# Performance work log

Measured on AMD Instinct MI355X. Metric: run time of the kernel, lower is better.

Reference implementation:

```python
import jax, jax.numpy as jnp
import numpy as np

B = 8        # number of clouds
NP = 4096    # points per cloud
STRIDE = 4   # sampler stride -> NS = NP // STRIDE sampled centers per cloud
K = 32       # knn neighbours
NS = NP // STRIDE


def setup_inputs() -> dict:
    key = jax.random.key(0)
    k1, k2, k3, k4 = jax.random.split(key, 4)
    N = B * NP
    x = jax.random.normal(k1, (N, 64), dtype=jnp.float32)
    pos = jax.random.normal(k2, (N, 3), dtype=jnp.float32)
    batch = jnp.repeat(jnp.arange(B, dtype=jnp.int64), NP)
    d_in = 64 + 3
    W1 = jax.random.normal(k3, (d_in, 128), dtype=jnp.float32) / np.sqrt(d_in)
    b1 = jnp.zeros((128,), dtype=jnp.float32)
    W2 = jax.random.normal(k4, (128, 256), dtype=jnp.float32) / np.sqrt(128)
    b2 = jnp.zeros((256,), dtype=jnp.float32)
    return {"x": x, "pos": pos, "batch": batch, "W1": W1, "b1": b1, "W2": W2, "b2": b2}


def reference(x, pos, batch, W1, b1, W2, b2):
    # --- sampler: stride sampling per cloud (clouds are equal-sized, contiguous) ---
    pos_b = pos.reshape(B, NP, 3)
    idx_local = jnp.arange(0, NP, STRIDE)                       # [NS]
    idx = (idx_local[None, :] + jnp.arange(B)[:, None] * NP).reshape(-1)  # global sampled idx [B*NS]
    pos_s = pos_b[:, idx_local]                                 # [B, NS, 3]

    # --- neighbour_finder: knn within each cloud (batch-respecting via per-cloud blocks) ---
    # squared distances [B, NS, NP] without materializing [B,NS,NP,3]
    d2 = ((pos_s ** 2).sum(-1)[:, :, None]
          + (pos_b ** 2).sum(-1)[:, None, :]
          - 2.0 * jnp.einsum('bsd,bnd->bsn', pos_s, pos_b))
    _, nbr = jax.lax.top_k(-d2, K)                              # [B, NS, K] local neighbour idx
    col = (nbr + (jnp.arange(B) * NP)[:, None, None]).reshape(-1)  # global neighbour idx [E]

    # --- conv: PointNetConv -> MLP(concat(x_j, pos_j - pos_i)) then max over neighbours ---
    x_j = x[col].reshape(B, NS, K, -1)                          # [B, NS, K, 64]
    rel = pos[col].reshape(B, NS, K, 3) - pos_s[:, :, None, :]  # pos_j - pos_i
    feat = jnp.concatenate([x_j, rel], axis=-1)                 # [B, NS, K, 67]
    h = jax.nn.relu(feat @ W1 + b1)                             # [B, NS, K, 128]
    h = jax.nn.relu(h @ W2 + b2)                                # [B, NS, K, 256]
    x_out = h.max(axis=2).reshape(B * NS, -1)                   # [B*NS, 256]

    pos_out = pos_s.reshape(-1, 3)
    batch_out = batch[idx]
    return x_out, pos_out, batch_out, idx
```

## Files before the change

### kernel.cpp

```cpp
#include <hip/hip_runtime.h>
#include <hip/hip_bf16.h>

#define BB 8
#define NP 4096
#define STRIDE 4
#define KNN 32
#define NS (NP/STRIDE)
#define NQ (BB*NS)
#define DIN 67
#define H1N 128
#define H2N 256
#define WCAP 512

typedef __attribute__((ext_vector_type(8)))  short bf16x8;
typedef __attribute__((ext_vector_type(16))) float f32x16;
typedef __attribute__((ext_vector_type(8)))  short short8;

__device__ __forceinline__ unsigned int f2u(float f) {
    unsigned int b = __float_as_uint(f);
    return (b & 0x80000000u) ? ~b : (b | 0x80000000u);
}
__device__ __forceinline__ short f2bf(float f) {
    unsigned u = __float_as_uint(f);
    unsigned r = u + 0x7FFFu + ((u >> 16) & 1u);
    return (short)(r >> 16);
}

__global__ __launch_bounds__(256) void knn_kernel(const float* __restrict__ pos,
                                                  int* __restrict__ col,
                                                  float* __restrict__ out) {
    __shared__ __align__(16) unsigned long long surv[4 * WCAP];
    __shared__ unsigned int pvt[4];
    __shared__ int cnts[4];

    const int q    = blockIdx.x;
    const int b    = q >> 10;
    const int s    = q & (NS - 1);
    const int qi   = b * NP + s * STRIDE;
    const int t    = threadIdx.x;
    const int w    = t >> 6;
    const int lane = t & 63;

    if (t == 128) pvt[3] = 0xFFFFFFFFu;

    if (t < 5) {
        float* pos_out   = out + (size_t)NQ * H2N;
        float* batch_out = pos_out + (size_t)NQ * 3;
        float* idx_out   = batch_out + NQ;
        if (t < 3)       pos_out[q*3+t] = pos[qi*3+t];
        else if (t == 3) batch_out[q] = (float)b;
        else             idx_out[q]   = (float)qi;
    }

    const float qx = pos[qi*3+0], qy = pos[qi*3+1], qz = pos[qi*3+2];
    const float q2 = __fadd_rn(__fadd_rn(__fmul_rn(qx,qx), __fmul_rn(qy,qy)), __fmul_rn(qz,qz));

    const float* pb = pos + (size_t)b * NP * 3;
    unsigned int myk[16];
    #pragma unroll
    for (int i = 0; i < 4; ++i) {
        const int u = t + i * 256;
        const float4* pp = (const float4*)(pb + (size_t)u * 12);
        const float4 v0 = pp[0], v1 = pp[1], v2 = pp[2];
        const float px[4] = {v0.x, v0.w, v1.z, v2.y};
        const float py[4] = {v0.y, v1.x, v1.w, v2.z};
        const float pz[4] = {v0.z, v1.y, v2.x, v2.w};
        #pragma unroll
        for (int j = 0; j < 4; ++j) {
            const float p2 = __fadd_rn(__fadd_rn(__fmul_rn(px[j],px[j]), __fmul_rn(py[j],py[j])), __fmul_rn(pz[j],pz[j]));
            const float dt = __fadd_rn(__fadd_rn(__fmul_rn(qx,px[j]), __fmul_rn(qy,py[j])), __fmul_rn(qz,pz[j]));
            const float d2 = __fsub_rn(__fadd_rn(q2, p2), __fmul_rn(2.0f, dt));
            myk[i*4+j] = f2u(d2);
        }
    }

    if (t < 64) {
        const unsigned int mk = myk[0];
        int rank = 0;
        #pragma unroll
        for (int ss = 0; ss < 64; ++ss) {
            const unsigned int ks = (unsigned int)__shfl((int)mk, ss, 64);
            rank += (int)((ks < mk) | ((ks == mk) & (ss < t)));
        }
        if (rank == 1)  pvt[0] = mk;
        if (rank == 3)  pvt[1] = mk;
        if (rank == 8)  pvt[2] = mk;
    }
    __syncthreads();

    int level = 0;
    {
        const unsigned int T = pvt[0];
        int base = 0;
        #pragma unroll
        for (int i = 0; i < 16; ++i) {
            const bool p = (myk[i] <= T);
            const unsigned long long mask = __ballot(p);
            if (p) {
                const int off = base + (int)__popcll(mask & ((1ull << lane) - 1ull));
                if (off < WCAP) {
                    const int n = 4 * (t + (i >> 2) * 256) + (i & 3);
                    surv[(w << 9) + off] = ((unsigned long long)myk[i] << 32) | (unsigned int)n;
                }
            }
            base += (int)__popcll(mask);
        }
        if (lane == 0) cnts[w] = (base < WCAP) ? base : WCAP;
    }
    __syncthreads();

    int c0 = cnts[0], c1 = cnts[1], c2 = cnts[2], c3 = cnts[3];
    int C = c0 + c1 + c2 + c3;

    if (C < KNN) {
        for (level = 1; level < 4; ++level) {
            const unsigned int T = pvt[level];
            int cw = 0;
            #pragma unroll
            for (int i = 0; i < 16; ++i)
                cw += (int)__popcll(__ballot(myk[i] <= T));
            if (lane == 0) cnts[w] = cw;
            __syncthreads();
            C = cnts[0] + cnts[1] + cnts[2] + cnts[3];
            if (C >= KNN) break;
            __syncthreads();
        }
        __syncthreads();
        {
            const unsigned int T = pvt[level];
            int base = 0;
            #pragma unroll
            for (int i = 0; i < 16; ++i) {
                const bool p = (myk[i] <= T);
                const unsigned long long mask = __ballot(p);
                if (p) {
                    const int off = base + (int)__popcll(mask & ((1ull << lane) - 1ull));
                    if (off < WCAP) {
                        const int n = 4 * (t + (i >> 2) * 256) + (i & 3);
                        surv[(w << 9) + off] = ((unsigned long long)myk[i] << 32) | (unsigned int)n;
                    }
                }
                base += (int)__popcll(mask);
            }
            if (lane == 0) cnts[w] = (base < WCAP) ? base : WCAP;
        }
        __syncthreads();
        c0 = cnts[0]; c1 = cnts[1]; c2 = cnts[2]; c3 = cnts[3];
        C = c0 + c1 + c2 + c3;
    }

    const int s1 = c0, s2 = c0 + c1, s3 = c0 + c1 + c2;
    const int cseg[4] = {c0, c1, c2, c3};
    for (int j = t; j < C; j += 256) {
        const int seg = (int)(j >= s1) + (int)(j >= s2) + (int)(j >= s3);
        const int off = j - ((seg == 0) ? 0 : (seg == 1) ? s1 : (seg == 2) ? s2 : s3);
        const unsigned long long v = surv[(seg << 9) + off];
        int rk = 0;
        #pragma unroll 1
        for (int k = 0; k < 4; ++k) {
            const ulonglong2* sp2 = (const ulonglong2*)(surv + (k << 9));
            const int ck = cseg[k];
            const int ck2 = ck >> 1;
            #pragma unroll 4
            for (int ss = 0; ss < ck2; ++ss) {
                const ulonglong2 pr = sp2[ss];
                rk += (int)(pr.x < v) + (int)(pr.y < v);
            }
            if (ck & 1) rk += (int)(surv[(k << 9) + ck - 1] < v);
        }
        if (rk < KNN)
            col[q * KNN + rk] = b * NP + (int)(unsigned int)(v & 0xFFFFFFFFull);
    }
}

__global__ __launch_bounds__(64) void prep_w(const float* __restrict__ W1,
                                             const float* __restrict__ W2,
                                             short* __restrict__ W1T,
                                             short* __restrict__ W2T) {
    const int l = threadIdx.x;
    if (blockIdx.x < 20) {
        const int nt = blockIdx.x / 5, t = blockIdx.x % 5;
        const int c  = 32*nt + (l & 31);
        short8 v;
        #pragma unroll
        for (int b = 0; b < 8; ++b) {
            const int k = 16*t + 8*(l >> 5) + b;
            v[b] = (k < DIN) ? f2bf(W1[k * H1N + c]) : (short)0;
        }
        *(short8*)(W1T + ((size_t)(nt*5 + t) * 64 + l) * 8) = v;
    } else {
        const int bb = blockIdx.x - 20;
        const int nt = bb >> 3, t = bb & 7;
        const int c  = 32*nt + (l & 31);
        short8 v;
        #pragma unroll
        for (int b = 0; b < 8; ++b) {
            const int k = 16*t + 8*(l >> 5) + b;
            v[b] = f2bf(W2[k * H2N + c]);
        }
        *(short8*)(W2T + ((size_t)(nt*8 + t) * 64 + l) * 8) = v;
    }
}

__global__ __launch_bounds__(256, 2) void mlp_mfma(const float* __restrict__ x,
                                                   const float* __restrict__ pos,
                                                   const int* __restrict__ col,
                                                   const float* __restrict__ b1,
                                                   const float* __restrict__ b2,
                                                   const short* __restrict__ W1T,
                                                   const short* __restrict__ W2T,
                                                   float* __restrict__ out) {
    __shared__ __align__(16) short feat[128 * 80];
    __shared__ __align__(16) short h1s [128 * 128];

    const int q0 = blockIdx.x * 4;
    const int t  = threadIdx.x;
    const int w  = t >> 6, l = t & 63;

    {
        const int row  = t >> 1, part = t & 1;
        const int q    = q0 + (row >> 5);
        const int c    = col[q * KNN + (row & 31)];
        const float4* xr = (const float4*)(x + (size_t)c * 64 + part * 32);
        short* fr = feat + row * 80 + part * 32;
        #pragma unroll
        for (int i = 0; i < 8; ++i) {
            const float4 v = xr[i];
            *(int*)(fr + i * 4 + 0) = (int)((unsigned short)f2bf(v.x) | ((unsigned)(unsigned short)f2bf(v.y) << 16));
            *(int*)(fr + i * 4 + 2) = (int)((unsigned short)f2bf(v.z) | ((unsigned)(unsigned short)f2bf(v.w) << 16));
        }
        if (part == 0) {
            const int b  = q >> 10;
            const int qi = b * NP + (q & (NS - 1)) * STRIDE;
            short8 o;
            o[0] = f2bf(pos[c*3+0] - pos[qi*3+0]);
            o[1] = f2bf(pos[c*3+1] - pos[qi*3+1]);
            o[2] = f2bf(pos[c*3+2] - pos[qi*3+2]);
            o[3] = 0; o[4] = 0; o[5] = 0; o[6] = 0; o[7] = 0;
            *(short8*)(feat + row * 80 + 64) = o;
            short8 z = {0,0,0,0,0,0,0,0};
            *(short8*)(feat + row * 80 + 72) = z;
        }
    }
    __syncthreads();

    const int lr = l & 31;
    const int lh = l >> 5;

    {
        bf16x8 w1f[20];
        #pragma unroll
        for (int i = 0; i < 20; ++i)
            w1f[i] = *(const bf16x8*)(W1T + ((size_t)i * 64 + l) * 8);

        bf16x8 a1[5];
        #pragma unroll
        for (int kt = 0; kt < 5; ++kt) {
            const int row = 32*w + lr;
            a1[kt] = *(const bf16x8*)(feat + row * 80 + 16*kt + 8*lh);
        }

        #pragma unroll
        for (int nt = 0; nt < 4; ++nt) {
            const float bv = b1[32*nt + lr];
            f32x16 acc;
            #pragma unroll
            for (int r = 0; r < 16; ++r) acc[r] = bv;
            #pragma unroll
            for (int kt = 0; kt < 5; ++kt)
                acc = __builtin_amdgcn_mfma_f32_32x32x16_bf16(a1[kt], w1f[nt*5 + kt], acc, 0, 0, 0);
            #pragma unroll
            for (int r = 0; r < 16; ++r) {
                const int i   = (r & 3) + 8*(r >> 2) + 4*lh;
                const int row = 32*w + i;
                const int c   = 32*nt + lr;
                const int adr = row * 128 + ((((c >> 3) ^ (row & 15)) << 3) | (c & 7));
                h1s[adr] = f2bf(fmaxf(acc[r], 0.0f));
            }
        }
    }
    __syncthreads();

    {
        bf16x8 a2[8];
        #pragma unroll
        for (int kt = 0; kt < 8; ++kt) {
            const int row  = 32*w + lr;
            const int slot = 2*kt + lh;
            a2[kt] = *(const bf16x8*)(h1s + row * 128 + ((slot ^ (row & 15)) << 3));
        }

        f32x16 acc[8];
        #pragma unroll
        for (int nt = 0; nt < 8; ++nt)
            #pragma unroll
            for (int r = 0; r < 16; ++r) acc[nt][r] = 0.0f;

        bf16x8 cur[8];
        #pragma unroll
        for (int kt = 0; kt < 8; ++kt)
            cur[kt] = *(const bf16x8*)(W2T + ((size_t)kt * 64 + l) * 8);

        #pragma unroll
        for (int nt = 0; nt < 8; ++nt) {
            bf16x8 nxt[8];
            if (nt < 7) {
                #pragma unroll
                for (int kt = 0; kt < 8; ++kt)
                    nxt[kt] = *(const bf16x8*)(W2T + ((size_t)((nt+1)*8 + kt) * 64 + l) * 8);
            }
            #pragma unroll
            for (int kt = 0; kt < 8; ++kt)
                acc[nt] = __builtin_amdgcn_mfma_f32_32x32x16_bf16(a2[kt], cur[kt], acc[nt], 0, 0, 0);
            #pragma unroll
            for (int kt = 0; kt < 8; ++kt) cur[kt] = nxt[kt];
        }

        const int q = q0 + w;
        #pragma unroll
        for (int nt = 0; nt < 8; ++nt) {
            float m = acc[nt][0];
            #pragma unroll
            for (int r = 1; r < 16; ++r) m = fmaxf(m, acc[nt][r]);
            m = fmaxf(m, __shfl_xor(m, 32, 64));
            m = fmaxf(m + b2[32*nt + lr], 0.0f);
            if (l < 32) out[(size_t)q * H2N + 32*nt + l] = m;
        }
    }
}

extern "C" void kernel_launch(void* const* d_in, const int* in_sizes, int n_in,
                              void* d_out, int out_size, void* d_ws, size_t ws_size,
                              hipStream_t stream) {
    const float* x   = (const float*)d_in[0];
    const float* pos = (const float*)d_in[1];
    const float* W1  = (const float*)d_in[3];
    const float* b1  = (const float*)d_in[4];
    const float* W2  = (const float*)d_in[5];
    const float* b2  = (const float*)d_in[6];
    float* out = (float*)d_out;

    char* ws   = (char*)d_ws;
    int*  col  = (int*)ws;
    short* W1T = (short*)(ws + 1048576);
    short* W2T = (short*)(ws + 1048576 + 20480);

    prep_w<<<84, 64, 0, stream>>>(W1, W2, W1T, W2T);
    knn_kernel<<<NQ, 256, 0, stream>>>(pos, col, out);
    mlp_mfma<<<NQ/4, 256, 0, stream>>>(x, pos, col, b1, b2, W1T, W2T, out);
}
```

Before: 154.9 us.

## Process two KNN queries per block with per-wave pivots and padded rank loops

Each KNN block now handles two adjacent sampled queries, so the loaded cloud positions and their squared norms are reused for both distance computations, and the grid is halved. Pivot thresholds are now computed in every wave and combined with a max across waves, which gives a more conservative threshold and lets the first-pass count of survivors reach K more often. The ranking loop pads each segment with sentinel values to a multiple of eight, removing the odd tail. This doubles register and shared-memory use per block and adds an occupancy hint, which may limit concurrency.

```diff
diff --git a/kernel.cpp b/kernel.cpp
--- a/kernel.cpp
+++ b/kernel.cpp
@@ -25,38 +25,45 @@
     unsigned r = u + 0x7FFFu + ((u >> 16) & 1u);
     return (short)(r >> 16);
 }
-
-__global__ __launch_bounds__(256) void knn_kernel(const float* __restrict__ pos,
-                                                  int* __restrict__ col,
-                                                  float* __restrict__ out) {
-    __shared__ __align__(16) unsigned long long surv[4 * WCAP];
-    __shared__ unsigned int pvt[4];
-    __shared__ int cnts[4];
-
-    const int q    = blockIdx.x;
-    const int b    = q >> 10;
-    const int s    = q & (NS - 1);
-    const int qi   = b * NP + s * STRIDE;
+__device__ __forceinline__ unsigned int umax4(unsigned int a, unsigned int b,
+                                              unsigned int c, unsigned int d) {
+    unsigned int ab = a > b ? a : b, cd = c > d ? c : d;
+    return ab > cd ? ab : cd;
+}
+
+__global__ __launch_bounds__(256, 4) void knn_kernel(const float* __restrict__ pos,
+                                                     int* __restrict__ col,
+                                                     float* __restrict__ out) {
+    __shared__ __align__(16) unsigned long long surv[8 * WCAP];
+    __shared__ unsigned int pvt[2][4][4];
+    __shared__ int cnts[8];
+
     const int t    = threadIdx.x;
     const int w    = t >> 6;
     const int lane = t & 63;
-
-    if (t == 128) pvt[3] = 0xFFFFFFFFu;
-
-    if (t < 5) {
+    const int q0   = blockIdx.x * 2;
+    const int b    = q0 >> 10;
+    const int s0   = q0 & (NS - 1);
+    const int qi0  = b * NP + s0 * STRIDE;
+    const int qi1  = qi0 + STRIDE;
+
+    if (w < 2 && lane < 5) {
+        const int qq = q0 + w, qiq = w ? qi1 : qi0;
         float* pos_out   = out + (size_t)NQ * H2N;
         float* batch_out = pos_out + (size_t)NQ * 3;
         float* idx_out   = batch_out + NQ;
-        if (t < 3)       pos_out[q*3+t] = pos[qi*3+t];
-        else if (t == 3) batch_out[q] = (float)b;
-        else             idx_out[q]   = (float)qi;
-    }
-
-    const float qx = pos[qi*3+0], qy = pos[qi*3+1], qz = pos[qi*3+2];
-    const float q2 = __fadd_rn(__fadd_rn(__fmul_rn(qx,qx), __fmul_rn(qy,qy)), __fmul_rn(qz,qz));
+        if (lane < 3)       pos_out[qq*3+lane] = pos[qiq*3+lane];
+        else if (lane == 3) batch_out[qq] = (float)b;
+        else                idx_out[qq]   = (float)qiq;
+    }
+
+    const float qx0 = pos[qi0*3+0], qy0 = pos[qi0*3+1], qz0 = pos[qi0*3+2];
+    const float qx1 = pos[qi1*3+0], qy1 = pos[qi1*3+1], qz1 = pos[qi1*3+2];
+    const float q20 = __fadd_rn(__fadd_rn(__fmul_rn(qx0,qx0), __fmul_rn(qy0,qy0)), __fmul_rn(qz0,qz0));
+    const float q21 = __fadd_rn(__fadd_rn(__fmul_rn(qx1,qx1), __fmul_rn(qy1,qy1)), __fmul_rn(qz1,qz1));
 
     const float* pb = pos + (size_t)b * NP * 3;
-    unsigned int myk[16];
+    unsigned int myk0[16], myk1[16];
     #pragma unroll
     for (int i = 0; i < 4; ++i) {
         const int u = t + i * 256;
@@ -68,108 +75,150 @@
         #pragma unroll
         for (int j = 0; j < 4; ++j) {
             const float p2 = __fadd_rn(__fadd_rn(__fmul_rn(px[j],px[j]), __fmul_rn(py[j],py[j])), __fmul_rn(pz[j],pz[j]));
-            const float dt = __fadd_rn(__fadd_rn(__fmul_rn(qx,px[j]), __fmul_rn(qy,py[j])), __fmul_rn(qz,pz[j]));
-            const float d2 = __fsub_rn(__fadd_rn(q2, p2), __fmul_rn(2.0f, dt));
-            myk[i*4+j] = f2u(d2);
-        }
-    }
-
-    if (t < 64) {
-        const unsigned int mk = myk[0];
-        int rank = 0;
+            const float dt0 = __fadd_rn(__fadd_rn(__fmul_rn(qx0,px[j]), __fmul_rn(qy0,py[j])), __fmul_rn(qz0,pz[j]));
+            const float dt1 = __fadd_rn(__fadd_rn(__fmul_rn(qx1,px[j]), __fmul_rn(qy1,py[j])), __fmul_rn(qz1,pz[j]));
+            myk0[i*4+j] = f2u(__fsub_rn(__fadd_rn(q20, p2), __fmul_rn(2.0f, dt0)));
+            myk1[i*4+j] = f2u(__fsub_rn(__fadd_rn(q21, p2), __fmul_rn(2.0f, dt1)));
+        }
+    }
+
+    {
+        const unsigned int mk0 = myk0[0], mk1 = myk1[0];
+        int r0 = 0, r1 = 0;
         #pragma unroll
         for (int ss = 0; ss < 64; ++ss) {
-            const unsigned int ks = (unsigned int)__shfl((int)mk, ss, 64);
-            rank += (int)((ks < mk) | ((ks == mk) & (ss < t)));
-        }
-        if (rank == 1)  pvt[0] = mk;
-        if (rank == 3)  pvt[1] = mk;
-        if (rank == 8)  pvt[2] = mk;
+            const unsigned int k0 = (unsigned int)__shfl((int)mk0, ss, 64);
+            const unsigned int k1 = (unsigned int)__shfl((int)mk1, ss, 64);
+            r0 += (int)((k0 < mk0) | ((k0 == mk0) & (ss < lane)));
+            r1 += (int)((k1 < mk1) | ((k1 == mk1) & (ss < lane)));
+        }
+        if (r0 == 1)  pvt[0][0][w] = mk0;
+        if (r0 == 3)  pvt[0][1][w] = mk0;
+        if (r0 == 8)  pvt[0][2][w] = mk0;
+        if (r0 == 31) pvt[0][3][w] = mk0;
+        if (r1 == 1)  pvt[1][0][w] = mk1;
+        if (r1 == 3)  pvt[1][1][w] = mk1;
+        if (r1 == 8)  pvt[1][2][w] = mk1;
+        if (r1 == 31) pvt[1][3][w] = mk1;
     }
     __syncthreads();
 
-    int level = 0;
-    {
-        const unsigned int T = pvt[0];
+    int cw0, cw1;
+    {
+        const unsigned int T0 = umax4(pvt[0][0][0], pvt[0][0][1], pvt[0][0][2], pvt[0][0][3]);
+        const unsigned int T1 = umax4(pvt[1][0][0], pvt[1][0][1], pvt[1][0][2], pvt[1][0][3]);
+        int b0 = 0, b1 = 0;
+        #pragma unroll
+        for (int i = 0; i < 16; ++i) {
+            const int n = 4 * (t + (i >> 2) * 256) + (i & 3);
+            const bool p0 = (myk0[i] <= T0);
+            const bool p1 = (myk1[i] <= T1);
+            const unsigned long long m0 = __ballot(p0);
+            const unsigned long long m1 = __ballot(p1);
+            if (p0) {
+                const int off = b0 + (int)__popcll(m0 & ((1ull << lane) - 1ull));
+                if (off < WCAP) surv[(w << 9) + off] = ((unsigned long long)myk0[i] << 32) | (unsigned int)n;
+            }
+            if (p1) {
+                const int off = b1 + (int)__popcll(m1 & ((1ull << lane) - 1ull));
+                if (off < WCAP) surv[2048 + (w << 9) + off] = ((unsigned long long)myk1[i] << 32) | (unsigned int)n;
+            }
+            b0 += (int)__popcll(m0);
+            b1 += (int)__popcll(m1);
+        }
+        cw0 = (b0 < WCAP) ? b0 : WCAP;
+        cw1 = (b1 < WCAP) ? b1 : WCAP;
+    }
+    if (lane == 0) { cnts[w] = cw0; cnts[4 + w] = cw1; }
+    __syncthreads();
+
+    int C0 = cnts[0] + cnts[1] + cnts[2] + cnts[3];
+    int C1 = cnts[4] + cnts[5] + cnts[6] + cnts[7];
+
+    int lvl = 0;
+    while (C0 < KNN && lvl < 3) {
+        ++lvl;
+        const unsigned int T = umax4(pvt[0][lvl][0], pvt[0][lvl][1], pvt[0][lvl][2], pvt[0][lvl][3]);
+        __syncthreads();
         int base = 0;
         #pragma unroll
         for (int i = 0; i < 16; ++i) {
-            const bool p = (myk[i] <= T);
-            const unsigned long long mask = __ballot(p);
+            const bool p = (myk0[i] <= T);
+            const unsigned long long m = __ballot(p);
             if (p) {
-                const int off = base + (int)__popcll(mask & ((1ull << lane) - 1ull));
+                const int off = base + (int)__popcll(m & ((1ull << lane) - 1ull));
                 if (off < WCAP) {
                     const int n = 4 * (t + (i >> 2) * 256) + (i & 3);
-                    surv[(w << 9) + off] = ((unsigned long long)myk[i] << 32) | (unsigned int)n;
+                    surv[(w << 9) + off] = ((unsigned long long)myk0[i] << 32) | (unsigned int)n;
                 }
             }
-            base += (int)__popcll(mask);
-        }
-        if (lane == 0) cnts[w] = (base < WCAP) ? base : WCAP;
+            base += (int)__popcll(m);
+        }
+        cw0 = (base < WCAP) ? base : WCAP;
+        if (lane == 0) cnts[w] = cw0;
+        __syncthreads();
+        C0 = cnts[0] + cnts[1] + cnts[2] + cnts[3];
+    }
+    lvl = 0;
+    while (C1 < KNN && lvl < 3) {
+        ++lvl;
+        const unsigned int T = umax4(pvt[1][lvl][0], pvt[1][lvl][1], pvt[1][lvl][2], pvt[1][lvl][3]);
+        __syncthreads();
+        int base = 0;
+        #pragma unroll
+        for (int i = 0; i < 16; ++i) {
+            const bool p = (myk1[i] <= T);
+            const unsigned long long m = __ballot(p);
+            if (p) {
+                const int off = base + (int)__popcll(m & ((1ull << lane) - 1ull));
+                if (off < WCAP) {
+                    const int n = 4 * (t + (i >> 2) * 256) + (i & 3);
+                    surv[2048 + (w << 9) + off] = ((unsigned long long)myk1[i] << 32) | (unsigned int)n;
+                }
+            }
+            base += (int)__popcll(m);
+        }
+        cw1 = (base < WCAP) ? base : WCAP;
+        if (lane == 0) cnts[4 + w] = cw1;
+        __syncthreads();
+        C1 = cnts[4] + cnts[5] + cnts[6] + cnts[7];
+    }
+
+    {
+        const int p0 = (cw0 + 7) & ~7;
+        for (int i = cw0 + lane; i < p0; i += 64) surv[(w << 9) + i] = ~0ull;
+        const int p1 = (cw1 + 7) & ~7;
+        for (int i = cw1 + lane; i < p1; i += 64) surv[2048 + (w << 9) + i] = ~0ull;
     }
     __syncthreads();
 
-    int c0 = cnts[0], c1 = cnts[1], c2 = cnts[2], c3 = cnts[3];
-    int C = c0 + c1 + c2 + c3;
-
-    if (C < KNN) {
-        for (level = 1; level < 4; ++level) {
-            const unsigned int T = pvt[level];
-            int cw = 0;
-            #pragma unroll
-            for (int i = 0; i < 16; ++i)
-                cw += (int)__popcll(__ballot(myk[i] <= T));
-            if (lane == 0) cnts[w] = cw;
-            __syncthreads();
-            C = cnts[0] + cnts[1] + cnts[2] + cnts[3];
-            if (C >= KNN) break;
-            __syncthreads();
-        }
-        __syncthreads();
-        {
-            const unsigned int T = pvt[level];
-            int base = 0;
-            #pragma unroll
-            for (int i = 0; i < 16; ++i) {
-                const bool p = (myk[i] <= T);
-                const unsigned long long mask = __ballot(p);
-                if (p) {
-                    const int off = base + (int)__popcll(mask & ((1ull << lane) - 1ull));
-                    if (off < WCAP) {
-                        const int n = 4 * (t + (i >> 2) * 256) + (i & 3);
-                        surv[(w << 9) + off] = ((unsigned long long)myk[i] << 32) | (unsigned int)n;
-                    }
+    {
+        const int half = w >> 1;
+        const int tl   = t & 127;
+        const unsigned long long* sb = surv + (half << 11);
+        const int* cn = cnts + (half << 2);
+        const int cs0 = cn[0], cs1 = cn[1], cs2 = cn[2], cs3 = cn[3];
+        const int Cq  = cs0 + cs1 + cs2 + cs3;
+        const int e1 = cs0, e2 = cs0 + cs1, e3 = cs0 + cs1 + cs2;
+        const int qq = q0 + half;
+        for (int j = tl; j < Cq; j += 128) {
+            const int seg = (int)(j >= e1) + (int)(j >= e2) + (int)(j >= e3);
+            const int off = j - ((seg == 0) ? 0 : (seg == 1) ? e1 : (seg == 2) ? e2 : e3);
+            const unsigned long long v = sb[(seg << 9) + off];
+            int rk = 0;
+            #pragma unroll 1
+            for (int k = 0; k < 4; ++k) {
+                const int np = ((cn[k] + 7) & ~7) >> 1;
+                const ulonglong2* sp = (const ulonglong2*)(sb + (k << 9));
+                #pragma unroll 4
+                for (int ss = 0; ss < np; ++ss) {
+                    const ulonglong2 pr = sp[ss];
+                    rk += (int)(pr.x < v) + (int)(pr.y < v);
                 }
-                base += (int)__popcll(mask);
-            }
-            if (lane == 0) cnts[w] = (base < WCAP) ? base : WCAP;
-        }
-        __syncthreads();
-        c0 = cnts[0]; c1 = cnts[1]; c2 = cnts[2]; c3 = cnts[3];
-        C = c0 + c1 + c2 + c3;
-    }
-
-    const int s1 = c0, s2 = c0 + c1, s3 = c0 + c1 + c2;
-    const int cseg[4] = {c0, c1, c2, c3};
-    for (int j = t; j < C; j += 256) {
-        const int seg = (int)(j >= s1) + (int)(j >= s2) + (int)(j >= s3);
-        const int off = j - ((seg == 0) ? 0 : (seg == 1) ? s1 : (seg == 2) ? s2 : s3);
-        const unsigned long long v = surv[(seg << 9) + off];
-        int rk = 0;
-        #pragma unroll 1
-        for (int k = 0; k < 4; ++k) {
-            const ulonglong2* sp2 = (const ulonglong2*)(surv + (k << 9));
-            const int ck = cseg[k];
-            const int ck2 = ck >> 1;
-            #pragma unroll 4
-            for (int ss = 0; ss < ck2; ++ss) {
-                const ulonglong2 pr = sp2[ss];
-                rk += (int)(pr.x < v) + (int)(pr.y < v);
-            }
-            if (ck & 1) rk += (int)(surv[(k << 9) + ck - 1] < v);
-        }
-        if (rk < KNN)
-            col[q * KNN + rk] = b * NP + (int)(unsigned int)(v & 0xFFFFFFFFull);
+            }
+            if (rk < KNN)
+                col[qq * KNN + rk] = b * NP + (int)(unsigned int)(v & 0xFFFFFFFFull);
+        }
     }
 }
 
@@ -346,6 +395,6 @@
     short* W2T = (short*)(ws + 1048576 + 20480);
 
     prep_w<<<84, 64, 0, stream>>>(W1, W2, W1T, W2T);
-    knn_kernel<<<NQ, 256, 0, stream>>>(pos, col, out);
+    knn_kernel<<<NQ/2, 256, 0, stream>>>(pos, col, out);
     mlp_mfma<<<NQ/4, 256, 0, stream>>>(x, pos, col, b1, b2, W1T, W2T, out);
 }
```

Measured after the change: 226.9 us. 1.46x slower.
